# Kernel optimization log

Hardware: AMD Instinct MI355X
Metric: run time of the kernel (lower is better)

Reference implementation:

```python
import jax, jax.numpy as jnp
import numpy as np

DEPTH = 4
HEADS = 8
DIM = 512
MLP = 2048
EPS = 1e-5


def layernorm(x, w, b):
    m = x.mean(-1, keepdims=True)
    v = x.var(-1, keepdims=True)
    return (x - m) * jax.lax.rsqrt(v + EPS) * w + b


def setup_inputs() -> dict:
    key = jax.random.key(0)
    ks = jax.random.split(key, 6)
    s = 0.02
    x = jax.random.normal(ks[0], (4, 2048, DIM), dtype=jnp.float32)
    return {
        "x": x,
        "ln1_w": jnp.ones((DEPTH, DIM), jnp.float32),
        "ln1_b": jnp.zeros((DEPTH, DIM), jnp.float32),
        "qkv_w": jax.random.normal(ks[1], (DEPTH, 3 * DIM, DIM), jnp.float32) * s,
        "proj_w": jax.random.normal(ks[2], (DEPTH, DIM, DIM), jnp.float32) * s,
        "proj_b": jnp.zeros((DEPTH, DIM), jnp.float32),
        "ln2_w": jnp.ones((DEPTH, DIM), jnp.float32),
        "ln2_b": jnp.zeros((DEPTH, DIM), jnp.float32),
        "fc1_w": jax.random.normal(ks[3], (DEPTH, MLP, DIM), jnp.float32) * s,
        "fc1_b": jnp.zeros((DEPTH, MLP), jnp.float32),
        "fc2_w": jax.random.normal(ks[4], (DEPTH, DIM, MLP), jnp.float32) * s,
        "fc2_b": jnp.zeros((DEPTH, DIM), jnp.float32),
    }


def reference(x, ln1_w, ln1_b, qkv_w, proj_w, proj_b, ln2_w, ln2_b, fc1_w, fc1_b, fc2_w, fc2_b):
    B, N, C = x.shape
    Dh = C // HEADS
    scale = Dh ** (-0.5)
    for i in range(DEPTH):
        # PreNorm attention block
        h = layernorm(x, ln1_w[i], ln1_b[i])
        qkv = (h @ qkv_w[i].T).reshape(B, N, 3, HEADS, Dh).transpose(2, 0, 3, 1, 4)
        q, k, v = qkv[0], qkv[1], qkv[2]          # [B,H,N,Dh]
        attn = jax.nn.softmax(jnp.einsum('bhnd,bhmd->bhnm', q, k) * scale, axis=-1)
        o = jnp.einsum('bhnm,bhmd->bhnd', attn, v).transpose(0, 2, 1, 3).reshape(B, N, C)
        x = o @ proj_w[i].T + proj_b[i] + x
        # PreNorm FFN block (exact erf GELU, matching torch nn.GELU default)
        h = layernorm(x, ln2_w[i], ln2_b[i])
        h = jax.nn.gelu(h @ fc1_w[i].T + fc1_b[i], approximate=False)
        x = h @ fc2_w[i].T + fc2_b[i] + x
    return x
```

## Files before the change

kernel.cpp:

```cpp
#include <hip/hip_runtime.h>
#include <hip/hip_bf16.h>
#include <math.h>

#define NB 4
#define HEADS 8
#define DIM 512
#define MLP 2048
#define NT 2048
#define DH 64
#define M_TOK (NB*NT)

typedef __bf16 bf16;
typedef __bf16 bf16x2 __attribute__((ext_vector_type(2)));
typedef __bf16 bf16x4 __attribute__((ext_vector_type(4)));
typedef __bf16 bf16x8 __attribute__((ext_vector_type(8)));
typedef float f32x4 __attribute__((ext_vector_type(4)));

__device__ __forceinline__ void gl_lds16(const void* g, void* l) {
    __builtin_amdgcn_global_load_lds((const __attribute__((address_space(1))) unsigned int*)g,
                                     (__attribute__((address_space(3))) unsigned int*)l, 16, 0, 0);
}

#define BARRIER() do { __builtin_amdgcn_s_barrier(); asm volatile("" ::: "memory"); } while(0)
#define WAIT_VM4() asm volatile("s_waitcnt vmcnt(4)" ::: "memory")
#define WAIT_VM0() asm volatile("s_waitcnt vmcnt(0)" ::: "memory")

__device__ __forceinline__ float fast_gelu(float u) {
    float u2 = u * u;
    float y  = u * __builtin_fmaf(u2, 0.044715f, 1.0f);
    float e  = exp2f(y * 2.3021839f);
    float r  = __builtin_amdgcn_rcpf(e + 1.0f);
    return u - u * r;
}

__global__ void cvt_bf16_kernel(const float* __restrict__ src, bf16* __restrict__ dst, int n) {
    int i = (blockIdx.x * 256 + threadIdx.x) * 4;
    if (i < n) {
        float4 v = *(const float4*)(src + i);
        bf16x4 o;
        o[0] = (bf16)v.x; o[1] = (bf16)v.y; o[2] = (bf16)v.z; o[3] = (bf16)v.w;
        *(bf16x4*)(dst + i) = o;
    }
}

__global__ void ln_kernel(const float* __restrict__ X, const float* __restrict__ gam,
                          const float* __restrict__ bet, bf16* __restrict__ out) {
    int w = threadIdx.x >> 6, l = threadIdx.x & 63;
    long row = (long)blockIdx.x * 4 + w;
    const float* xp = X + row * DIM + l * 8;
    float4 a = *(const float4*)xp;
    float4 b = *(const float4*)(xp + 4);
    float s1 = a.x + a.y + a.z + a.w + b.x + b.y + b.z + b.w;
    float s2 = a.x*a.x + a.y*a.y + a.z*a.z + a.w*a.w + b.x*b.x + b.y*b.y + b.z*b.z + b.w*b.w;
#pragma unroll
    for (int off = 32; off; off >>= 1) { s1 += __shfl_xor(s1, off); s2 += __shfl_xor(s2, off); }
    float mean = s1 * (1.f / 512.f);
    float var  = s2 * (1.f / 512.f) - mean * mean;
    float rstd = rsqrtf(var + 1e-5f);
    float4 g0 = *(const float4*)(gam + l * 8), g1 = *(const float4*)(gam + l * 8 + 4);
    float4 b0 = *(const float4*)(bet + l * 8), b1 = *(const float4*)(bet + l * 8 + 4);
    bf16x8 o;
    o[0] = (bf16)((a.x - mean) * rstd * g0.x + b0.x);
    o[1] = (bf16)((a.y - mean) * rstd * g0.y + b0.y);
    o[2] = (bf16)((a.z - mean) * rstd * g0.z + b0.z);
    o[3] = (bf16)((a.w - mean) * rstd * g0.w + b0.w);
    o[4] = (bf16)((b.x - mean) * rstd * g1.x + b1.x);
    o[5] = (bf16)((b.y - mean) * rstd * g1.y + b1.y);
    o[6] = (bf16)((b.z - mean) * rstd * g1.z + b1.z);
    o[7] = (bf16)((b.w - mean) * rstd * g1.w + b1.w);
    *(bf16x8*)(out + row * DIM + l * 8) = o;
}

#define G_LOADA(AF, B_, MQ) do { \
  _Pragma("unroll") for (int mi_ = 0; mi_ < 2; ++mi_) \
  _Pragma("unroll") for (int kk_ = 0; kk_ < 2; ++kk_) { \
    int row_ = wr * 64 + ((MQ) * 2 + mi_) * 16 + c; \
    AF[mi_][kk_] = *(const bf16x8*)&Abuf[B_][row_ * 64 + (((kk_ * 64 + g * 16) ^ sw) >> 1)]; \
  } } while (0)

#define G_LOADB(BF, B_, NQ) do { \
  _Pragma("unroll") for (int ni_ = 0; ni_ < 2; ++ni_) \
  _Pragma("unroll") for (int kk_ = 0; kk_ < 2; ++kk_) { \
    int row_ = wc * 64 + ((NQ) * 2 + ni_) * 16 + c; \
    BF[ni_][kk_] = *(const bf16x8*)&Bbuf[B_][row_ * 64 + (((kk_ * 64 + g * 16) ^ sw) >> 1)]; \
  } } while (0)

#define G_MFMA(AF, BF, MQ, NQ) do { \
  __builtin_amdgcn_s_setprio(1); \
  _Pragma("unroll") for (int mi_ = 0; mi_ < 2; ++mi_) \
  _Pragma("unroll") for (int ni_ = 0; ni_ < 2; ++ni_) \
  _Pragma("unroll") for (int kk_ = 0; kk_ < 2; ++kk_) \
    acc[(MQ)*2+mi_][(NQ)*2+ni_] = __builtin_amdgcn_mfma_f32_16x16x32_bf16( \
        AF[mi_][kk_], BF[ni_][kk_], acc[(MQ)*2+mi_][(NQ)*2+ni_], 0, 0, 0); \
  __builtin_amdgcn_s_setprio(0); \
} while (0)

#define G_STAGE_A(J_, H_) do { int j_ = (J_); if (j_ < nkt) { \
  bf16* db_ = Abuf[j_ & 1]; const bf16* sb_ = Aptr + (size_t)j_ * 64 + coloff; \
  _Pragma("unroll") for (int q_ = 0; q_ < 2; ++q_) { \
    int rw_ = q_ * 64 + (H_) * 32 + (w << 3); \
    gl_lds16(sb_ + (size_t)(arow0 + rw_ + lr) * KN, db_ + rw_ * 64); \
  } } } while (0)

#define G_STAGE_B(J_, H_) do { int j_ = (J_); if (j_ < nkt) { \
  bf16* db_ = Bbuf[j_ & 1]; const bf16* sb_ = Wptr + (size_t)j_ * 64 + coloff; \
  _Pragma("unroll") for (int q_ = 0; q_ < 2; ++q_) { \
    int rw_ = q_ * 64 + (H_) * 32 + (w << 3); \
    gl_lds16(sb_ + (size_t)(bcol0 + rw_ + lr) * KN, db_ + rw_ * 64); \
  } } } while (0)

template<int EPI, int KN>
__global__ __launch_bounds__(256, 2) void gemm128(const bf16* __restrict__ Aptr,
                                                  const bf16* __restrict__ Wptr,
                                                  const float* __restrict__ bias,
                                                  const float* __restrict__ resid,
                                                  void* outp, int N, bf16* __restrict__ vtout) {
    __shared__ bf16 Abuf[2][128 * 64];
    __shared__ bf16 Bbuf[2][128 * 64];
    const int t = threadIdx.x, w = t >> 6, l = t & 63;
    const int wr = w >> 1, wc = w & 1, g = l >> 4, c = l & 15;
    const int sw = (c & 7) << 4;
    const int lr = l >> 3;
    const int coloff = ((l & 7) ^ lr) << 3;

    int nwg = gridDim.x, bid = blockIdx.x;
    int q8 = nwg >> 3, r8 = nwg & 7;
    int xcd = bid & 7, rank = bid >> 3;
    int swz = (xcd < r8) ? xcd * (q8 + 1) + rank : r8 * (q8 + 1) + (xcd - r8) * q8 + rank;
    int tiles_n = N >> 7;
    long arow0 = (long)(swz / tiles_n) * 128;
    long bcol0 = (long)(swz % tiles_n) * 128;

    const int nkt = KN / 64;
    const int niter = nkt / 2;
    f32x4 acc[4][4] = {};
    bf16x8 af[2][2], bn0[2][2], bn1[2][2];

    G_STAGE_A(0, 0); G_STAGE_B(0, 0); G_STAGE_A(0, 1); G_STAGE_B(0, 1);
    G_STAGE_A(1, 0); G_STAGE_B(1, 0);

#pragma unroll 1
    for (int tt = 0; tt < niter; ++tt) {
        const int J0 = 2 * tt, J1 = 2 * tt + 1;
        const bool last = (tt == niter - 1);
        WAIT_VM4(); BARRIER();
        G_LOADA(af, 0, 0); G_LOADB(bn0, 0, 0);
        G_STAGE_A(J0 + 1, 1);
        G_MFMA(af, bn0, 0, 0);
        BARRIER();
        G_LOADB(bn1, 0, 1);
        G_STAGE_B(J0 + 1, 1);
        G_MFMA(af, bn1, 0, 1);
        BARRIER();
        G_LOADA(af, 0, 1);
        G_STAGE_A(J0 + 2, 0);
        G_MFMA(af, bn0, 1, 0);
        BARRIER();
        G_STAGE_B(J0 + 2, 0);
        G_MFMA(af, bn1, 1, 1);
        BARRIER();
        if (last) { WAIT_VM0(); } else { WAIT_VM4(); }
        BARRIER();
        G_LOADA(af, 1, 0); G_LOADB(bn0, 1, 0);
        G_STAGE_A(J1 + 1, 1);
        G_MFMA(af, bn0, 0, 0);
        BARRIER();
        G_LOADB(bn1, 1, 1);
        G_STAGE_B(J1 + 1, 1);
        G_MFMA(af, bn1, 0, 1);
        BARRIER();
        G_LOADA(af, 1, 1);
        G_STAGE_A(J1 + 2, 0);
        G_MFMA(af, bn0, 1, 0);
        BARRIER();
        G_STAGE_B(J1 + 2, 0);
        G_MFMA(af, bn1, 1, 1);
        BARRIER();
    }

    if constexpr (EPI == 0) {
        const int s = (int)(bcol0 >> 9);
        const float qscale = 0.18033688011112042f;
        if (s == 2) {
#pragma unroll
            for (int m = 0; m < 4; ++m)
#pragma unroll
                for (int n = 0; n < 4; ++n) {
                    int col = (int)(bcol0 + wc * 64 + n * 16 + c);
                    int d = col & 63, hh = (col >> 6) & 7;
                    long row = arow0 + wr * 64 + m * 16 + g * 4;
                    int bb = (int)(row >> 11), nn = (int)(row & 2047);
                    bf16x4 o4;
#pragma unroll
                    for (int r = 0; r < 4; ++r) o4[r] = (bf16)acc[m][n][r];
                    *(bf16x4*)(vtout + ((long)(bb * 8 + hh) * 64 + d) * 2048 + nn) = o4;
                }
        } else {
            const float sc = (s == 0) ? qscale : 1.0f;
#pragma unroll
            for (int m = 0; m < 4; ++m)
#pragma unroll
                for (int n = 0; n < 4; ++n) {
                    int col = (int)(bcol0 + wc * 64 + n * 16 + c);
                    int hh = (col >> 6) & 7, d = col & 63;
                    long row = arow0 + wr * 64 + m * 16 + g * 4;
#pragma unroll
                    for (int r = 0; r < 4; ++r) {
                        long rr = row + r;
                        int bb = (int)(rr >> 11), nn = (int)(rr & 2047);
                        ((bf16*)outp)[(((long)(s * NB + bb) * HEADS + hh) * NT + nn) * DH + d] =
                            (bf16)(acc[m][n][r] * sc);
                    }
                }
        }
    } else {
#pragma unroll
        for (int m = 0; m < 4; ++m)
#pragma unroll
            for (int n = 0; n < 4; ++n) {
                long row = arow0 + wr * 64 + m * 16 + g * 4;
                long col = bcol0 + wc * 64 + n * 16 + c;
#pragma unroll
                for (int r = 0; r < 4; ++r) {
                    long rr = row + r;
                    float u = acc[m][n][r] + bias[col];
                    ((bf16*)outp)[rr * N + col] = (bf16)fast_gelu(u);
                }
            }
    }
}

template<int KN, int NOUT, int EPI>
__global__ __launch_bounds__(256, 2) void gemm_n64(const bf16* __restrict__ A,
                                                   const bf16* __restrict__ W,
                                                   const float* __restrict__ bias,
                                                   const float* __restrict__ resid,
                                                   void* __restrict__ outp) {
    __shared__ bf16 As[128 * 64];
    __shared__ bf16 Bs[64 * 64];
    const int t = threadIdx.x, w = t >> 6, l = t & 63;
    const int wr = w >> 1, wc = w & 1, g = l >> 4, c = l & 15;
    const long arow0 = (long)blockIdx.y * 128;
    const long bcol0 = (long)blockIdx.x * 64;
    f32x4 acc[4][2] = {};
    const int lrow = l >> 3, lcol = (l & 7) * 8;
    const bf16* Ab = A + (arow0 + lrow) * (long)KN + lcol;
    const bf16* Wb = W + (bcol0 + lrow) * (long)KN + lcol;
    for (int k0 = 0; k0 < KN; k0 += 64) {
#pragma unroll
        for (int q = 0; q < 4; ++q)
            gl_lds16(Ab + (long)(w * 4 + q) * 8 * KN + k0, &As[(w * 4 + q) * 512]);
#pragma unroll
        for (int q = 0; q < 2; ++q)
            gl_lds16(Wb + (long)(w * 2 + q) * 8 * KN + k0, &Bs[(w * 2 + q) * 512]);
        __syncthreads();
#pragma unroll
        for (int kk = 0; kk < 2; ++kk) {
            bf16x8 afv[4], bfr[2];
#pragma unroll
            for (int m = 0; m < 4; ++m)
                afv[m] = *(const bf16x8*)&As[(wr * 64 + m * 16 + c) * 64 + kk * 32 + g * 8];
#pragma unroll
            for (int n = 0; n < 2; ++n)
                bfr[n] = *(const bf16x8*)&Bs[(wc * 32 + n * 16 + c) * 64 + kk * 32 + g * 8];
#pragma unroll
            for (int m = 0; m < 4; ++m)
#pragma unroll
                for (int n = 0; n < 2; ++n)
                    acc[m][n] = __builtin_amdgcn_mfma_f32_16x16x32_bf16(afv[m], bfr[n], acc[m][n], 0, 0, 0);
        }
        __syncthreads();
    }
#pragma unroll
    for (int m = 0; m < 4; ++m)
#pragma unroll
        for (int n = 0; n < 2; ++n) {
            long row = arow0 + wr * 64 + m * 16 + g * 4;
            long col = bcol0 + wc * 32 + n * 16 + c;
#pragma unroll
            for (int r = 0; r < 4; ++r) {
                long rr = row + r;
                float v = acc[m][n][r] + bias[col];
                if constexpr (EPI == 1) {
                    ((float*)outp)[rr * NOUT + col] = v + resid[rr * NOUT + col];
                } else {
                    ((bf16*)outp)[rr * NOUT + col] = (bf16)fast_gelu(v);
                }
            }
        }
}

#define NKT (NT / 64)

#define ATT_STAGE(J_, B_) do { \
    const bf16* ks_ = kbase + (size_t)(J_) * (64 * DH); \
    const bf16* vs_ = vbase + (J_) * 64; \
    gl_lds16(ks_,           &Ks[B_][(w * 8) * 64]); \
    gl_lds16(ks_ + 32 * DH, &Ks[B_][(32 + w * 8) * 64]); \
    gl_lds16(vs_,           &Vs[B_][(w * 8) * 64]); \
    gl_lds16(vs_ + 32 * NT, &Vs[B_][(32 + w * 8) * 64]); \
} while (0)

#define ATT_QK(B_, ST) do { \
    bf16x8 kf_[4][2]; \
    _Pragma("unroll") for (int kc = 0; kc < 4; ++kc) \
    _Pragma("unroll") for (int kk = 0; kk < 2; ++kk) \
        kf_[kc][kk] = *(const bf16x8*)&Ks[B_][(kc * 16 + c) * 64 + (((kk * 64 + g * 16) ^ xr) >> 1)]; \
    _Pragma("unroll") for (int kc = 0; kc < 4; ++kc) \
    _Pragma("unroll") for (int kk = 0; kk < 2; ++kk) \
        ST[kc] = __builtin_amdgcn_mfma_f32_16x16x32_bf16(kf_[kc][kk], qf[kk], ST[kc], 0, 0, 0); \
} while (0)

#define ATT_BODY(BUF, KT, SIN, SOUT) do { \
    bf16x8 vf[4][2]; \
    _Pragma("unroll") for (int dc = 0; dc < 4; ++dc) \
    _Pragma("unroll") for (int ks = 0; ks < 2; ++ks) \
        vf[dc][ks] = *(const bf16x8*)((const char*)&Vs[BUF][0] + (dc * 16 + c) * 128 + ((ks * 64 + g * 16) ^ xr)); \
    bf16x8 pf[2]; \
    _Pragma("unroll") for (int a = 0; a < 4; ++a) \
    _Pragma("unroll") for (int r = 0; r < 4; ++r) \
        pf[a >> 1][(a & 1) * 4 + r] = (bf16)exp2f(SIN[a][r]); \
    __syncthreads(); \
    if ((KT) + 2 < NKT) ATT_STAGE((KT) + 2, BUF); \
    _Pragma("unroll") for (int kc = 0; kc < 4; ++kc) SOUT[kc] = z4; \
    __builtin_amdgcn_s_setprio(1); \
    if ((KT) + 1 < NKT) ATT_QK((BUF) ^ 1, SOUT); \
    _Pragma("unroll") for (int ks = 0; ks < 2; ++ks) \
        sacc = __builtin_amdgcn_mfma_f32_16x16x32_bf16(ones8, pf[ks], sacc, 0, 0, 0); \
    _Pragma("unroll") for (int dc = 0; dc < 4; ++dc) \
    _Pragma("unroll") for (int ks = 0; ks < 2; ++ks) \
        oacc[dc] = __builtin_amdgcn_mfma_f32_16x16x32_bf16(vf[dc][ks], pf[ks], oacc[dc], 0, 0, 0); \
    __builtin_amdgcn_s_setprio(0); \
} while (0)

__global__ __launch_bounds__(256, 4) void attn_kernel(const bf16* __restrict__ qkv,
                                                      const bf16* __restrict__ vt,
                                                      bf16* __restrict__ O) {
    __shared__ bf16 Ks[2][64 * 64];
    __shared__ bf16 Vs[2][64 * 64];
    const int t = threadIdx.x, w = t >> 6, l = t & 63;
    const int g = l >> 4, c = l & 15;
    const int wg = blockIdx.x;
    const int xcd = wg & 7, rank = wg >> 3;
    const int bh = xcd + 8 * (rank >> 5);
    const int qt = rank & 31;
    const bf16* Qb = qkv + (long)bh * (NT * DH);
    const bf16* Kb = Qb + (long)(NB * HEADS) * (NT * DH);
    const bf16* Vtb = vt + (long)bh * (DH * NT);
    const int q0 = qt * 64 + w * 16;
    const int lr = l >> 3, lc = l & 7;
    const int sch = ((lc ^ lr) & 7) * 8;
    const int xr = (c & 7) << 4;

    const bf16* kbase = Kb + (long)(w * 8 + lr) * DH + sch;
    const bf16* vbase = Vtb + (long)(w * 8 + lr) * NT + sch;

    bf16x8 qf[2];
#pragma unroll
    for (int kk = 0; kk < 2; ++kk)
        qf[kk] = *(const bf16x8*)(Qb + (long)(q0 + c) * DH + kk * 32 + g * 8);

    bf16x8 ones8;
#pragma unroll
    for (int j = 0; j < 8; ++j) ones8[j] = (bf16)1.0f;
    const f32x4 z4 = {};

    f32x4 oacc[4] = {};
    f32x4 sacc = {};
    f32x4 st0[4] = {}, st1[4];

    ATT_STAGE(0, 0);
    ATT_STAGE(1, 1);
    __syncthreads();
    ATT_QK(0, st0);

#pragma unroll 1
    for (int kt2 = 0; kt2 < NKT / 2; ++kt2) {
        ATT_BODY(0, kt2 * 2,     st0, st1);
        ATT_BODY(1, kt2 * 2 + 1, st1, st0);
    }

    float inv = 1.f / sacc[0];

    char* ol = (char*)&Ks[0][0] + w * 2048;
#pragma unroll
    for (int dc = 0; dc < 4; ++dc) {
        bf16x4 o4;
#pragma unroll
        for (int r = 0; r < 4; ++r) o4[r] = (bf16)(oacc[dc][r] * inv);
        *(bf16x4*)(ol + c * 128 + ((dc * 32 + g * 8) ^ xr)) = o4;
    }
    __builtin_amdgcn_s_waitcnt(0);
    const int orow = l >> 2, oc = (l & 3) * 16;
    const int bb = bh >> 3, hh = bh & 7;
    long tok = (long)bb * NT + q0 + orow;
    bf16* og = O + tok * DIM + hh * 64 + oc;
    const int xr2 = (orow & 7) << 4;
    bf16x8 v0 = *(const bf16x8*)(ol + orow * 128 + ((oc * 2) ^ xr2));
    bf16x8 v1 = *(const bf16x8*)(ol + orow * 128 + ((oc * 2 + 16) ^ xr2));
    *(bf16x8*)og = v0;
    *(bf16x8*)(og + 8) = v1;
}

extern "C" void kernel_launch(void* const* d_in, const int* in_sizes, int n_in,
                              void* d_out, int out_size, void* d_ws, size_t ws_size,
                              hipStream_t stream) {
    const float* x      = (const float*)d_in[0];
    const float* ln1_w  = (const float*)d_in[1];
    const float* ln1_b  = (const float*)d_in[2];
    const float* qkv_w  = (const float*)d_in[3];
    const float* proj_w = (const float*)d_in[4];
    const float* proj_b = (const float*)d_in[5];
    const float* ln2_w  = (const float*)d_in[6];
    const float* ln2_b  = (const float*)d_in[7];
    const float* fc1_w  = (const float*)d_in[8];
    const float* fc1_b  = (const float*)d_in[9];
    const float* fc2_w  = (const float*)d_in[10];
    const float* fc2_b  = (const float*)d_in[11];
    float* X = (float*)d_out;

    char* ws = (char*)d_ws;
    bf16* h_bf   = (bf16*)(ws);
    bf16* scr_bf = (bf16*)(ws + (size_t)(8  << 20));
    bf16* vt_bf  = (bf16*)(ws + (size_t)(32 << 20));
    bf16* o_bf   = (bf16*)(ws + (size_t)(40 << 20));
    bf16* w_qkv  = (bf16*)(ws + (size_t)(48 << 20));
    bf16* w_proj = w_qkv  + (size_t)4 * 1536 * 512;
    bf16* w_fc1  = w_proj + (size_t)4 * 512 * 512;
    bf16* w_fc2  = w_fc1  + (size_t)4 * 2048 * 512;

    {
        int n;
        n = 4 * 1536 * 512; cvt_bf16_kernel<<<n / 1024, 256, 0, stream>>>(qkv_w,  w_qkv,  n);
        n = 4 * 512 * 512;  cvt_bf16_kernel<<<n / 1024, 256, 0, stream>>>(proj_w, w_proj, n);
        n = 4 * 2048 * 512; cvt_bf16_kernel<<<n / 1024, 256, 0, stream>>>(fc1_w,  w_fc1,  n);
        n = 4 * 512 * 2048; cvt_bf16_kernel<<<n / 1024, 256, 0, stream>>>(fc2_w,  w_fc2,  n);
    }

    for (int i = 0; i < 4; ++i) {
        const float* Xin = (i == 0) ? x : X;
        ln_kernel<<<M_TOK / 4, 256, 0, stream>>>(Xin, ln1_w + i * 512, ln1_b + i * 512, h_bf);
        gemm128<0, 512><<<(M_TOK / 128) * (1536 / 128), 256, 0, stream>>>(
            h_bf, w_qkv + (size_t)i * 1536 * 512, nullptr, nullptr, scr_bf, 1536, vt_bf);
        attn_kernel<<<1024, 256, 0, stream>>>(scr_bf, vt_bf, o_bf);
        gemm_n64<512, 512, 1><<<dim3(8, 64), 256, 0, stream>>>(
            o_bf, w_proj + (size_t)i * 512 * 512, proj_b + i * 512, Xin, X);
        ln_kernel<<<M_TOK / 4, 256, 0, stream>>>(X, ln2_w + i * 512, ln2_b + i * 512, h_bf);
        gemm128<2, 512><<<(M_TOK / 128) * (2048 / 128), 256, 0, stream>>>(
            h_bf, w_fc1 + (size_t)i * 2048 * 512, fc1_b + i * 2048, nullptr, scr_bf, 2048, nullptr);
        gemm_n64<2048, 512, 1><<<dim3(8, 64), 256, 0, stream>>>(
            scr_bf, w_fc2 + (size_t)i * 512 * 2048, fc2_b + i * 512, X, X);
    }
}
```

Baseline: 710.3 us.

## Double-buffer LDS tiles in gemm_n64 with async prefetch two stages ahead

Converts the N=64 GEMM (used for proj and fc2 with residual epilogue) from a single-buffered load-sync-compute loop into a two-stage LDS ping-pong pipeline. Global-to-LDS loads for tile t+2 are issued after computing tile t, and partial vmcnt waits let the next tile's loads stay in flight during the MFMAs. It also raises wave priority around the MFMA block. LDS use doubles, which may affect the two-blocks-per-CU occupancy target.

```diff
diff --git a/kernel.cpp b/kernel.cpp
--- a/kernel.cpp
+++ b/kernel.cpp
@@ -23,6 +23,7 @@
 
 #define BARRIER() do { __builtin_amdgcn_s_barrier(); asm volatile("" ::: "memory"); } while(0)
 #define WAIT_VM4() asm volatile("s_waitcnt vmcnt(4)" ::: "memory")
+#define WAIT_VM6() asm volatile("s_waitcnt vmcnt(6)" ::: "memory")
 #define WAIT_VM0() asm volatile("s_waitcnt vmcnt(0)" ::: "memory")
 
 __device__ __forceinline__ float fast_gelu(float u) {
@@ -230,14 +231,40 @@
     }
 }
 
+#define N64_STAGE(T_, P_) do { \
+  _Pragma("unroll") for (int q_ = 0; q_ < 4; ++q_) \
+      gl_lds16(Ab + (long)(w * 4 + q_) * 8 * KN + (T_) * 64, &As[P_][(w * 4 + q_) * 512]); \
+  _Pragma("unroll") for (int q_ = 0; q_ < 2; ++q_) \
+      gl_lds16(Wb + (long)(w * 2 + q_) * 8 * KN + (T_) * 64, &Bs[P_][(w * 2 + q_) * 512]); \
+} while (0)
+
+#define N64_BODY(P_, T_) do { \
+    if ((T_) == nkt - 1) { WAIT_VM0(); } else { WAIT_VM6(); } \
+    BARRIER(); \
+    __builtin_amdgcn_s_setprio(1); \
+    _Pragma("unroll") for (int kk = 0; kk < 2; ++kk) { \
+        bf16x8 afv[4], bfr[2]; \
+        _Pragma("unroll") for (int m = 0; m < 4; ++m) \
+            afv[m] = *(const bf16x8*)&As[P_][(wr * 64 + m * 16 + c) * 64 + kk * 32 + g * 8]; \
+        _Pragma("unroll") for (int n = 0; n < 2; ++n) \
+            bfr[n] = *(const bf16x8*)&Bs[P_][(wc * 32 + n * 16 + c) * 64 + kk * 32 + g * 8]; \
+        _Pragma("unroll") for (int m = 0; m < 4; ++m) \
+        _Pragma("unroll") for (int n = 0; n < 2; ++n) \
+            acc[m][n] = __builtin_amdgcn_mfma_f32_16x16x32_bf16(afv[m], bfr[n], acc[m][n], 0, 0, 0); \
+    } \
+    __builtin_amdgcn_s_setprio(0); \
+    BARRIER(); \
+    if ((T_) + 2 < nkt) N64_STAGE((T_) + 2, P_); \
+} while (0)
+
 template<int KN, int NOUT, int EPI>
 __global__ __launch_bounds__(256, 2) void gemm_n64(const bf16* __restrict__ A,
                                                    const bf16* __restrict__ W,
                                                    const float* __restrict__ bias,
                                                    const float* __restrict__ resid,
                                                    void* __restrict__ outp) {
-    __shared__ bf16 As[128 * 64];
-    __shared__ bf16 Bs[64 * 64];
+    __shared__ bf16 As[2][128 * 64];
+    __shared__ bf16 Bs[2][64 * 64];
     const int t = threadIdx.x, w = t >> 6, l = t & 63;
     const int wr = w >> 1, wc = w & 1, g = l >> 4, c = l & 15;
     const long arow0 = (long)blockIdx.y * 128;
@@ -246,31 +273,18 @@
     const int lrow = l >> 3, lcol = (l & 7) * 8;
     const bf16* Ab = A + (arow0 + lrow) * (long)KN + lcol;
     const bf16* Wb = W + (bcol0 + lrow) * (long)KN + lcol;
-    for (int k0 = 0; k0 < KN; k0 += 64) {
-#pragma unroll
-        for (int q = 0; q < 4; ++q)
-            gl_lds16(Ab + (long)(w * 4 + q) * 8 * KN + k0, &As[(w * 4 + q) * 512]);
-#pragma unroll
-        for (int q = 0; q < 2; ++q)
-            gl_lds16(Wb + (long)(w * 2 + q) * 8 * KN + k0, &Bs[(w * 2 + q) * 512]);
-        __syncthreads();
-#pragma unroll
-        for (int kk = 0; kk < 2; ++kk) {
-            bf16x8 afv[4], bfr[2];
-#pragma unroll
-            for (int m = 0; m < 4; ++m)
-                afv[m] = *(const bf16x8*)&As[(wr * 64 + m * 16 + c) * 64 + kk * 32 + g * 8];
-#pragma unroll
-            for (int n = 0; n < 2; ++n)
-                bfr[n] = *(const bf16x8*)&Bs[(wc * 32 + n * 16 + c) * 64 + kk * 32 + g * 8];
-#pragma unroll
-            for (int m = 0; m < 4; ++m)
-#pragma unroll
-                for (int n = 0; n < 2; ++n)
-                    acc[m][n] = __builtin_amdgcn_mfma_f32_16x16x32_bf16(afv[m], bfr[n], acc[m][n], 0, 0, 0);
-        }
-        __syncthreads();
-    }
+    const int nkt = KN / 64;
+
+    N64_STAGE(0, 0);
+    N64_STAGE(1, 1);
+
+#pragma unroll 1
+    for (int t2 = 0; t2 < nkt / 2; ++t2) {
+        const int T0 = t2 * 2;
+        N64_BODY(0, T0);
+        N64_BODY(1, T0 + 1);
+    }
+
 #pragma unroll
     for (int m = 0; m < 4; ++m)
 #pragma unroll
```

New measurement: 715.6 us. Within noise of the previous version (+0.8%).
